# Performance work log

Measured on AMD Instinct MI355X. Metric: run time of the kernel, lower is better.

## Reference

```python
import jax, jax.numpy as jnp
import numpy as np

B, S, H = 32, 64, 512
ATT = 128


def _window_index_tables(seq_len):
    # Enumerate all contiguous windows of size 2..S, same set (order-independent
    # for the softmax-weighted sum) as the torch double loop.
    starts, ends = [], []
    for w in range(2, seq_len + 1):
        for s in range(0, seq_len - w + 1):
            starts.append(s)
            ends.append(s + w)
    starts = np.asarray(starts, np.int32)
    ends = np.asarray(ends, np.int32)
    widths = ends - starts
    ks = np.floor(np.log2(widths)).astype(np.int32)  # sparse-table level per window
    e2 = ends - (1 << ks)                            # second gather position
    return starts, e2, ks


def setup_inputs() -> dict:
    key = jax.random.key(0)
    k0, k1, k2, k3, k4 = jax.random.split(key, 5)
    return {
        "lstm_out": jax.random.normal(k0, (B, S, H), dtype=jnp.float32),
        "W1": jax.random.normal(k1, (H, ATT), dtype=jnp.float32) * 0.05,
        "b1": jax.random.normal(k2, (ATT,), dtype=jnp.float32) * 0.05,
        "W2": jax.random.normal(k3, (ATT, 1), dtype=jnp.float32) * 0.05,
        "b2": jax.random.normal(k4, (1,), dtype=jnp.float32) * 0.05,
    }


def reference(lstm_out, W1, b1, W2, b2):
    b, s, h = lstm_out.shape
    # Sparse table: M[k][:, i] = max over lstm_out[:, i : i+2^k] (clipped to s).
    n_levels = int(np.floor(np.log2(s))) + 1
    tables = [lstm_out]
    for k in range(1, n_levels):
        half = 1 << (k - 1)
        prev = tables[-1]
        shifted = jnp.concatenate(
            [prev[:, half:], jnp.full((b, half, h), -jnp.inf, prev.dtype)], axis=1)
        tables.append(jnp.maximum(prev, shifted))
    Mstack = jnp.stack(tables)  # [K, B, S, H]

    starts, e2, ks = _window_index_tables(s)
    # Range max of each window = max of two overlapping power-of-two blocks.
    pooled = jnp.maximum(Mstack[ks, :, starts], Mstack[ks, :, e2])  # [n_win, B, H]
    pooled = jnp.transpose(pooled, (1, 0, 2))  # [B, n_win, H]

    hid = jax.nn.relu(jnp.einsum("bnh,ha->bna", pooled, W1) + b1)
    scores = jnp.einsum("bna,ao->bno", hid, W2) + b2  # [B, n_win, 1]
    attn = jax.nn.softmax(scores, axis=1)
    return jnp.sum(attn * pooled, axis=1)  # [B, H]
```

## Files before the change

kernel.cpp:

```cpp
#include <hip/hip_runtime.h>
#include <stdint.h>

typedef unsigned short u16;
typedef unsigned int u32;

#define B_    32
#define S_    64
#define H_    512
#define ATT_  128
#define NWIN  2016
#define NLEV  7

typedef __bf16 bf16x8 __attribute__((ext_vector_type(8)));
typedef float  f32x4  __attribute__((ext_vector_type(4)));

__device__ __forceinline__ float asf(u32 i) {
  union { u32 i; float f; } v; v.i = i; return v.f;
}
__device__ __forceinline__ u32 asu(float f) {
  union { float f; u32 i; } v; v.f = f; return v.i;
}
__device__ __forceinline__ float bf2f(u16 u) { return asf(((u32)u) << 16); }
__device__ __forceinline__ u16 f2bf(float f) {
  u32 i = asu(f);
  i += 0x7fffu + ((i >> 16) & 1u);
  return (u16)(i >> 16);
}
__device__ __forceinline__ u32 bfmax2(u32 a, u32 b) {
  float a0 = asf(a << 16), a1 = asf(a & 0xffff0000u);
  float b0 = asf(b << 16), b1 = asf(b & 0xffff0000u);
  u32 m0 = asu(fmaxf(a0, b0)), m1 = asu(fmaxf(a1, b1));
  return (m1 & 0xffff0000u) | (m0 >> 16);
}
__device__ __forceinline__ uint4 bfmax8(uint4 a, uint4 b) {
  uint4 m;
  m.x = bfmax2(a.x, b.x); m.y = bfmax2(a.y, b.y);
  m.z = bfmax2(a.z, b.z); m.w = bfmax2(a.w, b.w);
  return m;
}

__launch_bounds__(256)
__global__ void k01_init(const float* __restrict__ lstm, const float* __restrict__ W1,
                         u16* __restrict__ table, u16* __restrict__ w1t,
                         u16* __restrict__ widx) {
  int bid = blockIdx.x, tid = threadIdx.x;
  __shared__ u16 bufA[64 * 64], bufB[64 * 64];
  if (bid < 256) {
    int hc = bid & 7, b = bid >> 3;
    const float* src = lstm + (size_t)b * S_ * H_ + hc * 64;
    u16* tb = table + (size_t)b * NLEV * S_ * H_ + hc * 64;
    for (int t = tid; t < 64 * 16; t += 256) {
      int r = t >> 4, c4 = t & 15;
      float4 f = *reinterpret_cast<const float4*>(src + r * H_ + c4 * 4);
      ushort4 u;
      u.x = f2bf(f.x); u.y = f2bf(f.y); u.z = f2bf(f.z); u.w = f2bf(f.w);
      *reinterpret_cast<ushort4*>(&bufA[r * 64 + c4 * 4]) = u;
      *reinterpret_cast<ushort4*>(tb + r * H_ + c4 * 4) = u;
    }
    u16* pa = bufA; u16* pb = bufB;
    for (int k = 1; k < NLEV; ++k) {
      __syncthreads();
      int half = 1 << (k - 1);
      u16* dst_g = tb + k * S_ * H_;
      for (int t = tid; t < 64 * 16; t += 256) {
        int r = t >> 4, c4 = t & 15;
        int r2 = r + half; if (r2 > 63) r2 = 63;
        uint2 a  = *reinterpret_cast<const uint2*>(&pa[r  * 64 + c4 * 4]);
        uint2 bq = *reinterpret_cast<const uint2*>(&pa[r2 * 64 + c4 * 4]);
        uint2 m; m.x = bfmax2(a.x, bq.x); m.y = bfmax2(a.y, bq.y);
        *reinterpret_cast<uint2*>(&pb[r * 64 + c4 * 4]) = m;
        *reinterpret_cast<uint2*>(dst_g + r * H_ + c4 * 4) = m;
      }
      u16* tmp = pa; pa = pb; pb = tmp;
    }
  } else {
    int gb = bid - 256;
    if (gb == 0) {
      for (int n = tid; n < NWIN; n += 256) {
        int w = 2, rem = n;
        while (rem >= 65 - w) { rem -= 65 - w; ++w; }
        int s = rem;
        int k = 31 - __clz(w);
        int e2 = s + w - (1 << k);
        widx[n] = (u16)(s | (e2 << 6) | (k << 12));
      }
    }
    for (int q = tid; q < 2048; q += 256) {
      int idx = gb * 2048 + q;
      int n = idx >> 9, kq = idx & 511;
      w1t[idx] = f2bf(W1[kq * ATT_ + n]);
    }
  }
}

__launch_bounds__(256, 3)
__global__ void k2_scores(const u16* __restrict__ table, const u16* __restrict__ w1t,
                          const float* __restrict__ b1, const float* __restrict__ w2,
                          const u16* __restrict__ widx, float* __restrict__ scores) {
  const int b = blockIdx.y, mt = blockIdx.x;
  __shared__ u16 As[96 * 72];
  __shared__ u16 Bs[128 * 72];
  __shared__ u16 widx_l[96];
  __shared__ float b1s[128], w2s[128], sc[96];
  int tid = threadIdx.x;
  if (tid < 96) { widx_l[tid] = widx[mt * 96 + tid]; sc[tid] = 0.f; }
  if (tid < 128) { b1s[tid] = b1[tid]; w2s[tid] = w2[tid]; }
  __syncthreads();

  const u16* tb = table + (size_t)b * NLEV * S_ * H_;
  int ar[3], ac[3];
  const u16 *apa[3], *apb[3];
#pragma unroll
  for (int i = 0; i < 3; ++i) {
    int t = tid + i * 256; ar[i] = t >> 3; ac[i] = t & 7;
    int pk = widx_l[ar[i]];
    int s = pk & 63, e2 = (pk >> 6) & 63, lv = pk >> 12;
    apa[i] = tb + (lv * S_ + s) * H_ + ac[i] * 8;
    apb[i] = tb + (lv * S_ + e2) * H_ + ac[i] * 8;
  }
  int bn[4], bc[4];
#pragma unroll
  for (int j = 0; j < 4; ++j) {
    int t = tid + j * 256; bn[j] = t >> 3; bc[j] = t & 7;
  }

  uint4 ra[3], rb[3], rB[4];
#define ISSUE(KK) do { \
  _Pragma("unroll") for (int i = 0; i < 3; ++i) { \
    ra[i] = *reinterpret_cast<const uint4*>(apa[i] + (KK)); \
    rb[i] = *reinterpret_cast<const uint4*>(apb[i] + (KK)); } \
  _Pragma("unroll") for (int j = 0; j < 4; ++j) \
    rB[j] = *reinterpret_cast<const uint4*>(w1t + bn[j] * H_ + (KK) + bc[j] * 8); \
} while (0)

  ISSUE(0);

  int wid = tid >> 6, lane = tid & 63;
  int wm = wid & 1, wn = wid >> 1;
  int lrow = lane & 15, quad = lane >> 4;

  f32x4 acc[3][4];
#pragma unroll
  for (int i = 0; i < 3; ++i)
#pragma unroll
    for (int j = 0; j < 4; ++j) acc[i][j] = (f32x4){0.f, 0.f, 0.f, 0.f};

  for (int kc = 0; kc < 8; ++kc) {
    uint4 mA[3];
#pragma unroll
    for (int i = 0; i < 3; ++i) mA[i] = bfmax8(ra[i], rb[i]);
    __syncthreads();
#pragma unroll
    for (int i = 0; i < 3; ++i)
      *reinterpret_cast<uint4*>(&As[ar[i] * 72 + ac[i] * 8]) = mA[i];
#pragma unroll
    for (int j = 0; j < 4; ++j)
      *reinterpret_cast<uint4*>(&Bs[bn[j] * 72 + bc[j] * 8]) = rB[j];
    __syncthreads();
    if (kc < 7) ISSUE((kc + 1) * 64);
#pragma unroll
    for (int ks = 0; ks < 64; ks += 32) {
      bf16x8 af[3], bfr[4];
#pragma unroll
      for (int i = 0; i < 3; ++i)
        af[i] = *reinterpret_cast<const bf16x8*>(&As[(wm * 48 + i * 16 + lrow) * 72 + ks + quad * 8]);
#pragma unroll
      for (int j = 0; j < 4; ++j)
        bfr[j] = *reinterpret_cast<const bf16x8*>(&Bs[(wn * 64 + j * 16 + lrow) * 72 + ks + quad * 8]);
#pragma unroll
      for (int i = 0; i < 3; ++i)
#pragma unroll
        for (int j = 0; j < 4; ++j)
          acc[i][j] = __builtin_amdgcn_mfma_f32_16x16x32_bf16(af[i], bfr[j], acc[i][j], 0, 0, 0);
    }
  }
#undef ISSUE

#pragma unroll
  for (int i = 0; i < 3; ++i) {
#pragma unroll
    for (int r = 0; r < 4; ++r) {
      float p = 0.f;
#pragma unroll
      for (int j = 0; j < 4; ++j) {
        int n = wn * 64 + j * 16 + lrow;
        float v = acc[i][j][r] + b1s[n];
        p += (v > 0.f ? v : 0.f) * w2s[n];
      }
      p += __shfl_xor(p, 1, 16);
      p += __shfl_xor(p, 2, 16);
      p += __shfl_xor(p, 4, 16);
      p += __shfl_xor(p, 8, 16);
      if (lrow == 0) atomicAdd(&sc[wm * 48 + i * 16 + quad * 4 + r], p);
    }
  }
  __syncthreads();
  if (tid < 96) scores[b * NWIN + mt * 96 + tid] = sc[tid];
}

__launch_bounds__(256)
__global__ void k34_out(const u16* __restrict__ table, const float* __restrict__ scores,
                        const u16* __restrict__ widx, float* __restrict__ out) {
  int hc = blockIdx.x, b = blockIdx.y, tid = threadIdx.x;
  __shared__ u16 Tl[6 * 64 * 32];
  __shared__ float attn_l[NWIN];
  __shared__ u16 widx_l[NWIN];
  __shared__ float red[8][32];
  __shared__ float wredM[4], wredS[4];
  const u16* tb = table + (size_t)b * NLEV * S_ * H_ + S_ * H_;
  int h0 = hc * 32;
  int lane = tid & 63, wid = tid >> 6;

  for (int t = tid; t < 6 * 64 * 4; t += 256) {
    int row = t >> 2, c = t & 3;
    uint4 v = *reinterpret_cast<const uint4*>(tb + row * H_ + h0 + c * 8);
    *reinterpret_cast<uint4*>(&Tl[row * 32 + c * 8]) = v;
  }
  for (int n = tid; n < NWIN; n += 256) widx_l[n] = widx[n];

  float mx = -1e30f;
  for (int n = tid; n < NWIN; n += 256) {
    float v = scores[b * NWIN + n];
    attn_l[n] = v;
    mx = fmaxf(mx, v);
  }
#pragma unroll
  for (int off = 32; off > 0; off >>= 1) mx = fmaxf(mx, __shfl_xor(mx, off, 64));
  if (lane == 0) wredM[wid] = mx;
  __syncthreads();
  mx = fmaxf(fmaxf(wredM[0], wredM[1]), fmaxf(wredM[2], wredM[3]));
  float sum = 0.f;
  for (int n = tid; n < NWIN; n += 256) {
    float e = __expf(attn_l[n] - mx);
    attn_l[n] = e;
    sum += e;
  }
#pragma unroll
  for (int off = 32; off > 0; off >>= 1) sum += __shfl_xor(sum, off, 64);
  if (lane == 0) wredS[wid] = sum;
  __syncthreads();
  float inv = 1.f / (wredS[0] + wredS[1] + wredS[2] + wredS[3]);

  int h = tid & 31, g = tid >> 5;
  float acc = 0.f;
  for (int n = g * 252; n < g * 252 + 252; ++n) {
    int pk = widx_l[n];
    int s = pk & 63, e2 = (pk >> 6) & 63, lv = pk >> 12;
    float va = bf2f(Tl[((lv - 1) * 64 + s) * 32 + h]);
    float vb = bf2f(Tl[((lv - 1) * 64 + e2) * 32 + h]);
    acc += attn_l[n] * fmaxf(va, vb);
  }
  red[g][h] = acc;
  __syncthreads();
  if (tid < 32) {
    float s2 = 0.f;
#pragma unroll
    for (int g2 = 0; g2 < 8; ++g2) s2 += red[g2][tid];
    out[b * H_ + h0 + tid] = s2 * inv;
  }
}

extern "C" void kernel_launch(void* const* d_in, const int* in_sizes, int n_in,
                              void* d_out, int out_size, void* d_ws, size_t ws_size,
                              hipStream_t stream) {
  const float* lstm = (const float*)d_in[0];
  const float* W1   = (const float*)d_in[1];
  const float* b1   = (const float*)d_in[2];
  const float* W2   = (const float*)d_in[3];
  float* out = (float*)d_out;

  char* ws = (char*)d_ws;
  u16*   widx   = (u16*)(ws + 0);
  u16*   w1t    = (u16*)(ws + 4096);
  u16*   table  = (u16*)(ws + 135168);
  float* scores = (float*)(ws + 14815232);

  k01_init <<<288, 256, 0, stream>>>(lstm, W1, table, w1t, widx);
  k2_scores<<<dim3(21, B_), 256, 0, stream>>>(table, w1t, b1, W2, widx, scores);
  k34_out  <<<dim3(16, B_), 256, 0, stream>>>(table, scores, widx, out);
}
```

Before: 133.2 us.

## Stage two sparse-table levels in LDS and gather window rows from shared memory

Each block now loads a contiguous 128-row slab of the sparse table (two adjacent levels starting at the first window's level) into LDS. It then builds the pooled A tile by gathering and max-ing rows from LDS, instead of issuing two scattered global loads per A row. This relies on the 96 windows of a tile spanning at most two levels. It adds about 18KB of LDS, an extra barrier per k-chunk, and removes the 3-blocks occupancy hint, so occupancy may drop.

Result: slower. 163.6 us (+22.8%).

```diff
diff --git a/kernel.cpp b/kernel.cpp
--- a/kernel.cpp
+++ b/kernel.cpp
@@ -93,11 +93,12 @@
   }
 }
 
-__launch_bounds__(256, 3)
+__launch_bounds__(256)
 __global__ void k2_scores(const u16* __restrict__ table, const u16* __restrict__ w1t,
                           const float* __restrict__ b1, const float* __restrict__ w2,
                           const u16* __restrict__ widx, float* __restrict__ scores) {
   const int b = blockIdx.y, mt = blockIdx.x;
+  __shared__ u16 Ts[128 * 72];
   __shared__ u16 As[96 * 72];
   __shared__ u16 Bs[128 * 72];
   __shared__ u16 widx_l[96];
@@ -107,30 +108,40 @@
   if (tid < 128) { b1s[tid] = b1[tid]; w2s[tid] = w2[tid]; }
   __syncthreads();
 
-  const u16* tb = table + (size_t)b * NLEV * S_ * H_;
-  int ar[3], ac[3];
-  const u16 *apa[3], *apb[3];
+  const int lv_lo = widx_l[0] >> 12;
+  const u16* tb = table + (size_t)b * NLEV * S_ * H_ + (size_t)lv_lo * S_ * H_;
+
+  const u16* tsrc[4]; int tdst[4];
+#pragma unroll
+  for (int i = 0; i < 4; ++i) {
+    int t = tid + i * 256, row = t >> 3, c = t & 7;
+    tsrc[i] = tb + row * H_ + c * 8;
+    tdst[i] = row * 72 + c * 8;
+  }
+  const u16* bsrc[4]; int bdst[4];
+#pragma unroll
+  for (int j = 0; j < 4; ++j) {
+    int t = tid + j * 256, n = t >> 3, c = t & 7;
+    bsrc[j] = w1t + n * H_ + c * 8;
+    bdst[j] = n * 72 + c * 8;
+  }
+  int aS[3], aE[3], aD[3];
 #pragma unroll
   for (int i = 0; i < 3; ++i) {
-    int t = tid + i * 256; ar[i] = t >> 3; ac[i] = t & 7;
-    int pk = widx_l[ar[i]];
-    int s = pk & 63, e2 = (pk >> 6) & 63, lv = pk >> 12;
-    apa[i] = tb + (lv * S_ + s) * H_ + ac[i] * 8;
-    apb[i] = tb + (lv * S_ + e2) * H_ + ac[i] * 8;
-  }
-  int bn[4], bc[4];
-#pragma unroll
-  for (int j = 0; j < 4; ++j) {
-    int t = tid + j * 256; bn[j] = t >> 3; bc[j] = t & 7;
-  }
-
-  uint4 ra[3], rb[3], rB[4];
+    int t = tid + i * 256, r = t >> 3, c = t & 7;
+    int pk = widx_l[r];
+    int s = pk & 63, e2 = (pk >> 6) & 63, lv = (pk >> 12) - lv_lo;
+    aS[i] = (lv * 64 + s) * 72 + c * 8;
+    aE[i] = (lv * 64 + e2) * 72 + c * 8;
+    aD[i] = r * 72 + c * 8;
+  }
+
+  uint4 rT[4], rB[4];
 #define ISSUE(KK) do { \
-  _Pragma("unroll") for (int i = 0; i < 3; ++i) { \
-    ra[i] = *reinterpret_cast<const uint4*>(apa[i] + (KK)); \
-    rb[i] = *reinterpret_cast<const uint4*>(apb[i] + (KK)); } \
+  _Pragma("unroll") for (int i = 0; i < 4; ++i) \
+    rT[i] = *reinterpret_cast<const uint4*>(tsrc[i] + (KK)); \
   _Pragma("unroll") for (int j = 0; j < 4; ++j) \
-    rB[j] = *reinterpret_cast<const uint4*>(w1t + bn[j] * H_ + (KK) + bc[j] * 8); \
+    rB[j] = *reinterpret_cast<const uint4*>(bsrc[j] + (KK)); \
 } while (0)
 
   ISSUE(0);
@@ -146,16 +157,20 @@
     for (int j = 0; j < 4; ++j) acc[i][j] = (f32x4){0.f, 0.f, 0.f, 0.f};
 
   for (int kc = 0; kc < 8; ++kc) {
-    uint4 mA[3];
-#pragma unroll
-    for (int i = 0; i < 3; ++i) mA[i] = bfmax8(ra[i], rb[i]);
     __syncthreads();
 #pragma unroll
-    for (int i = 0; i < 3; ++i)
-      *reinterpret_cast<uint4*>(&As[ar[i] * 72 + ac[i] * 8]) = mA[i];
+    for (int i = 0; i < 4; ++i)
+      *reinterpret_cast<uint4*>(&Ts[tdst[i]]) = rT[i];
 #pragma unroll
     for (int j = 0; j < 4; ++j)
-      *reinterpret_cast<uint4*>(&Bs[bn[j] * 72 + bc[j] * 8]) = rB[j];
+      *reinterpret_cast<uint4*>(&Bs[bdst[j]]) = rB[j];
+    __syncthreads();
+#pragma unroll
+    for (int i = 0; i < 3; ++i) {
+      uint4 va = *reinterpret_cast<const uint4*>(&Ts[aS[i]]);
+      uint4 vb = *reinterpret_cast<const uint4*>(&Ts[aE[i]]);
+      *reinterpret_cast<uint4*>(&As[aD[i]]) = bfmax8(va, vb);
+    }
     __syncthreads();
     if (kc < 7) ISSUE((kc + 1) * 64);
 #pragma unroll
```
